# Performance work log

Measured on AMD Instinct MI355X. Metric: run time of the kernel, lower is better.

## Reference

```python
import jax, jax.numpy as jnp
import numpy as np

EPS = 0.0  # original torch code has no eps; exact division by L2 norm

def setup_inputs() -> dict:
    key = jax.random.key(0)
    k1, k2 = jax.random.split(key)
    N, D = 262144, 256
    query_emb = jax.random.normal(k1, (N, D), dtype=jnp.float32)
    doc_emb = jax.random.normal(k2, (N, D), dtype=jnp.float32)
    return {"query_emb": query_emb, "doc_emb": doc_emb}

def reference(query_emb, doc_emb):
    # L2-normalize rows, then per-row dot product.
    # Mathematically identical to diag(qn @ dn.T) in the torch module,
    # but computed in O(N*d) instead of materializing an NxN matrix.
    q_norm = jnp.linalg.norm(query_emb, axis=1, keepdims=True)
    d_norm = jnp.linalg.norm(doc_emb, axis=1, keepdims=True)
    qn = query_emb / q_norm
    dn = doc_emb / d_norm
    sim_score = jnp.sum(qn * dn, axis=1, keepdims=True)  # [N, 1]
    return sim_score
```

## Files before the change

kernel.cpp:

```cpp
#include <hip/hip_runtime.h>

typedef float fx4 __attribute__((ext_vector_type(4)));

constexpr int ROWS_PER_WAVE = 4;
constexpr int WAVES_PER_BLOCK = 4;

__global__ __launch_bounds__(256) void cosine_rows_kernel(
    const fx4* __restrict__ q4,
    const fx4* __restrict__ d4,
    float* __restrict__ out,
    int n_rows)
{
    const int wave = (blockIdx.x * blockDim.x + threadIdx.x) >> 6;
    const int lane = threadIdx.x & 63;
    const int g    = lane >> 4;
    const int c    = lane & 15;
    const int row  = wave * ROWS_PER_WAVE + g;
    if (row >= n_rows) return;

    const size_t base = (size_t)row * 64 + c;

    fx4 qv[4], dv[4];
    #pragma unroll
    for (int k = 0; k < 4; ++k)
        qv[k] = q4[base + 16 * k];
    #pragma unroll
    for (int k = 0; k < 4; ++k)
        dv[k] = d4[base + 16 * k];

    float qq = 0.0f, dd = 0.0f, qd = 0.0f;
    #pragma unroll
    for (int k = 0; k < 4; ++k) {
        qq += qv[k].x * qv[k].x + qv[k].y * qv[k].y +
              qv[k].z * qv[k].z + qv[k].w * qv[k].w;
        dd += dv[k].x * dv[k].x + dv[k].y * dv[k].y +
              dv[k].z * dv[k].z + dv[k].w * dv[k].w;
        qd += qv[k].x * dv[k].x + qv[k].y * dv[k].y +
              qv[k].z * dv[k].z + qv[k].w * dv[k].w;
    }

    #pragma unroll
    for (int off = 8; off > 0; off >>= 1) {
        qq += __shfl_xor(qq, off, 64);
        dd += __shfl_xor(dd, off, 64);
        qd += __shfl_xor(qd, off, 64);
    }

    if (c == 0) {
        __builtin_nontemporal_store(qd * rsqrtf(qq * dd), &out[row]);
    }
}

extern "C" void kernel_launch(void* const* d_in, const int* in_sizes, int n_in,
                              void* d_out, int out_size, void* d_ws, size_t ws_size,
                              hipStream_t stream) {
    const fx4* q4 = (const fx4*)d_in[0];
    const fx4* d4 = (const fx4*)d_in[1];
    float* out = (float*)d_out;

    const int D = 256;
    const int n_rows = in_sizes[0] / D;

    const int rows_per_block = WAVES_PER_BLOCK * ROWS_PER_WAVE;
    const int grid = (n_rows + rows_per_block - 1) / rows_per_block;

    cosine_rows_kernel<<<grid, 256, 0, stream>>>(q4, d4, out, n_rows);
}
```

Baseline: 494.2 us.

## Use grid-stride persistent waves with two row-groups per iteration and nontemporal loads

```diff
diff --git a/kernel.cpp b/kernel.cpp
--- a/kernel.cpp
+++ b/kernel.cpp
@@ -2,8 +2,9 @@
 
 typedef float fx4 __attribute__((ext_vector_type(4)));
 
-constexpr int ROWS_PER_WAVE = 4;
-constexpr int WAVES_PER_BLOCK = 4;
+constexpr int ROWS_PER_GROUP = 4;
+constexpr int GROUPS_PER_ITER = 2;
+constexpr int BLOCKS = 2048;
 
 __global__ __launch_bounds__(256) void cosine_rows_kernel(
     const fx4* __restrict__ q4,
@@ -11,43 +12,59 @@
     float* __restrict__ out,
     int n_rows)
 {
-    const int wave = (blockIdx.x * blockDim.x + threadIdx.x) >> 6;
-    const int lane = threadIdx.x & 63;
-    const int g    = lane >> 4;
-    const int c    = lane & 15;
-    const int row  = wave * ROWS_PER_WAVE + g;
-    if (row >= n_rows) return;
+    const int nwaves = (gridDim.x * blockDim.x) >> 6;
+    const int wave   = (blockIdx.x * blockDim.x + threadIdx.x) >> 6;
+    const int lane   = threadIdx.x & 63;
+    const int g      = lane >> 4;
+    const int c      = lane & 15;
 
-    const size_t base = (size_t)row * 64 + c;
+    const int total_groups = n_rows >> 2;
 
-    fx4 qv[4], dv[4];
-    #pragma unroll
-    for (int k = 0; k < 4; ++k)
-        qv[k] = q4[base + 16 * k];
-    #pragma unroll
-    for (int k = 0; k < 4; ++k)
-        dv[k] = d4[base + 16 * k];
+    for (int grp = wave * GROUPS_PER_ITER; grp < total_groups;
+         grp += nwaves * GROUPS_PER_ITER) {
 
-    float qq = 0.0f, dd = 0.0f, qd = 0.0f;
-    #pragma unroll
-    for (int k = 0; k < 4; ++k) {
-        qq += qv[k].x * qv[k].x + qv[k].y * qv[k].y +
-              qv[k].z * qv[k].z + qv[k].w * qv[k].w;
-        dd += dv[k].x * dv[k].x + dv[k].y * dv[k].y +
-              dv[k].z * dv[k].z + dv[k].w * dv[k].w;
-        qd += qv[k].x * dv[k].x + qv[k].y * dv[k].y +
-              qv[k].z * dv[k].z + qv[k].w * dv[k].w;
-    }
+        fx4 qv[GROUPS_PER_ITER][4], dv[GROUPS_PER_ITER][4];
+        #pragma unroll
+        for (int u = 0; u < GROUPS_PER_ITER; ++u) {
+            if (grp + u < total_groups) {
+                const int row = (grp + u) * ROWS_PER_GROUP + g;
+                const size_t base = (size_t)row * 64 + c;
+                #pragma unroll
+                for (int k = 0; k < 4; ++k)
+                    qv[u][k] = __builtin_nontemporal_load(&q4[base + 16 * k]);
+                #pragma unroll
+                for (int k = 0; k < 4; ++k)
+                    dv[u][k] = __builtin_nontemporal_load(&d4[base + 16 * k]);
+            }
+        }
 
-    #pragma unroll
-    for (int off = 8; off > 0; off >>= 1) {
-        qq += __shfl_xor(qq, off, 64);
-        dd += __shfl_xor(dd, off, 64);
-        qd += __shfl_xor(qd, off, 64);
-    }
+        #pragma unroll
+        for (int u = 0; u < GROUPS_PER_ITER; ++u) {
+            if (grp + u < total_groups) {
+                float qq = 0.0f, dd = 0.0f, qd = 0.0f;
+                #pragma unroll
+                for (int k = 0; k < 4; ++k) {
+                    qq += qv[u][k].x * qv[u][k].x + qv[u][k].y * qv[u][k].y +
+                          qv[u][k].z * qv[u][k].z + qv[u][k].w * qv[u][k].w;
+                    dd += dv[u][k].x * dv[u][k].x + dv[u][k].y * dv[u][k].y +
+                          dv[u][k].z * dv[u][k].z + dv[u][k].w * dv[u][k].w;
+                    qd += qv[u][k].x * dv[u][k].x + qv[u][k].y * dv[u][k].y +
+                          qv[u][k].z * dv[u][k].z + qv[u][k].w * dv[u][k].w;
+                }
 
-    if (c == 0) {
-        __builtin_nontemporal_store(qd * rsqrtf(qq * dd), &out[row]);
+                #pragma unroll
+                for (int off = 8; off > 0; off >>= 1) {
+                    qq += __shfl_xor(qq, off, 64);
+                    dd += __shfl_xor(dd, off, 64);
+                    qd += __shfl_xor(qd, off, 64);
+                }
+
+                if (c == 0) {
+                    const int row = (grp + u) * ROWS_PER_GROUP + g;
+                    __builtin_nontemporal_store(qd * rsqrtf(qq * dd), &out[row]);
+                }
+            }
+        }
     }
 }
 
@@ -61,8 +78,10 @@
     const int D = 256;
     const int n_rows = in_sizes[0] / D;
 
-    const int rows_per_block = WAVES_PER_BLOCK * ROWS_PER_WAVE;
-    const int grid = (n_rows + rows_per_block - 1) / rows_per_block;
+    const int total_groups = n_rows / ROWS_PER_GROUP;
+    const int waves_needed = (total_groups + GROUPS_PER_ITER - 1) / GROUPS_PER_ITER;
+    const int blocks_needed = (waves_needed + 3) / 4;
+    const int grid = min(BLOCKS, blocks_needed);
 
     cosine_rows_kernel<<<grid, 256, 0, stream>>>(q4, d4, out, n_rows);
 }
```

Result: faster. 471.2 us (-4.6%).
